# Optimization experiments

Hardware: AMD Instinct MI355X
Metric: run time of the kernel (lower is better)

## Reference

```python
import jax, jax.numpy as jnp
import numpy as np

T, B, D, H = 512, 128, 512, 512

def setup_inputs() -> dict:
    key = jax.random.key(0)
    k1, k2, k3, k4 = jax.random.split(key, 4)
    s_in = 1.0 / np.sqrt(D)
    s_h = 1.0 / np.sqrt(H)
    return {
        "x": jax.random.normal(k1, (T, B, D), dtype=jnp.float32),
        "resets": jax.random.randint(k2, (T, B), 0, 2) > 0,
        "h0": jnp.zeros((B, H), dtype=jnp.float32),  # GRUCell.initialize_carry -> zeros
        "Wi": jax.random.normal(k3, (D, 3 * H), dtype=jnp.float32) * s_in,  # [ir|iz|in]
        "bi": jnp.zeros((3 * H,), dtype=jnp.float32),
        "Wh": jax.random.normal(k4, (H, 3 * H), dtype=jnp.float32) * s_h,  # [hr|hz|hn]
        "bhn": jnp.zeros((H,), dtype=jnp.float32),
    }

def reference(x, resets, h0, Wi, bi, Wh, bhn):
    # Precompute all input-side gate projections in one big GEMM: [T,B,3H]
    xg = jnp.einsum('tbd,dk->tbk', x, Wi) + bi

    def step(h, inp):
        xg_t, reset_t = inp
        # reset masking: replace carry with fresh zero carry where episode resets
        h = jnp.where(reset_t[:, None], jnp.zeros_like(h), h)
        hg = h @ Wh  # [B,3H]
        xr, xz, xn = jnp.split(xg_t, 3, axis=-1)
        hr, hz, hn = jnp.split(hg, 3, axis=-1)
        r = jax.nn.sigmoid(xr + hr)
        z = jax.nn.sigmoid(xz + hz)
        n = jnp.tanh(xn + r * (hn + bhn))
        h_new = (1.0 - z) * n + z * h
        return h_new, h_new

    h_final, ys = jax.lax.scan(step, h0, (xg, resets))
    return h_final, ys
```

## Files before the change

kernel.cpp:

```cpp
#include <hip/hip_runtime.h>

typedef __attribute__((ext_vector_type(4))) float f32x4;
typedef __attribute__((ext_vector_type(8))) _Float16 f16x8;
typedef __attribute__((ext_vector_type(4))) _Float16 f16x4;
typedef unsigned short u16;
typedef unsigned int u32;
typedef unsigned long long u64;

#define XGCAP 34304
#define NXG 4096

__device__ __forceinline__ float sigm(float v){ return 1.0f / (1.0f + __expf(-v)); }
__device__ __forceinline__ float tanh_fast(float v){
  v = fminf(15.0f, fmaxf(-15.0f, v));
  float e = __expf(2.0f * v);
  return (e - 1.0f) / (e + 1.0f);
}
__device__ __forceinline__ void gload16(const void* g, void* l){
  __builtin_amdgcn_global_load_lds((const __attribute__((address_space(1))) void*)g,
                                   (__attribute__((address_space(3))) void*)l, 16, 0, 0);
}
__device__ __forceinline__ double aload(const double* p){
  return __hip_atomic_load(p, __ATOMIC_RELAXED, __HIP_MEMORY_SCOPE_AGENT);
}
__device__ __forceinline__ void astore(float* p, float v){
  __hip_atomic_store(p, v, __ATOMIC_RELAXED, __HIP_MEMORY_SCOPE_AGENT);
}
__device__ __forceinline__ u32 apoll(const u32* p){
  return __hip_atomic_load(p, __ATOMIC_RELAXED, __HIP_MEMORY_SCOPE_AGENT);
}
__device__ __forceinline__ void abump(u32* p, u32 v){
  __hip_atomic_fetch_add(p, v, __ATOMIC_RELAXED, __HIP_MEMORY_SCOPE_AGENT);
}
__device__ __forceinline__ float2 d2f2(double d){ union{double d; float2 f;} u; u.d = d; return u.f; }

__global__ __launch_bounds__(512) void prep_lists(
    const void* __restrict__ resets_raw, const float* __restrict__ h0,
    u32* __restrict__ rows, u32* __restrict__ off, int* __restrict__ nlists)
{
  __shared__ u32 bitmap[2048];
  __shared__ u16 lcnt[127*128];
  __shared__ u32 cnt[520];
  __shared__ u32 offs[521];
  __shared__ u32 cur[520];
  __shared__ int is_bytes, h0nz;
  const int tid = threadIdx.x;
  const int lane = tid & 63, wave = tid >> 6;
  for (int i = tid; i < 2048; i += 512) bitmap[i] = 0;
  for (int i = tid; i < 127*128; i += 512) lcnt[i] = 0;
  for (int i = tid; i < 520; i += 512){ cnt[i] = 0; cur[i] = 0; }
  if (tid == 0){ is_bytes = 0; h0nz = 0; }
  for (int i = tid; i < 64; i += 512) rows[65536 + i] = (2u << 16);
  __syncthreads();
  {
    const u32* w = (const u32*)resets_raw;
    int bad = 0;
    for (int i = tid; i < 4096; i += 512) bad |= (w[i] > 1u);
    if (bad) atomicOr(&is_bytes, 1);
  }
  {
    const u32* hw = (const u32*)h0;
    u32 o = 0;
    for (int i = tid; i < 65536; i += 512) o |= hw[i];
    if (o) atomicOr(&h0nz, 1);
  }
  __syncthreads();
  const bool h0zero = (h0nz == 0);
  if (is_bytes){
    const u32* wb = (const u32*)resets_raw;
    for (int i = tid; i < 16384; i += 512){
      u32 v = wb[i];
      u32 bits = ((v & 0xFFu) ? 1u : 0u) | (((v >> 8) & 0xFFu) ? 2u : 0u)
               | (((v >> 16) & 0xFFu) ? 4u : 0u) | (((v >> 24) & 0xFFu) ? 8u : 0u);
      if (bits) atomicOr(&bitmap[i >> 3], bits << ((i & 7) * 4));
    }
  } else {
    const u32* w = (const u32*)resets_raw;
    for (int r = 0; r < 128; ++r){
      u32 v = w[r * 512 + tid];
      u64 m = __ballot(v != 0u);
      if (lane == 0){
        int idx = r * 16 + wave * 2;
        bitmap[idx] = (u32)m; bitmap[idx + 1] = (u32)(m >> 32);
      }
    }
  }
  __syncthreads();
  if (tid < 128){
    const int b = tid;
    int depth = 0;
    for (int t = 0; t < 512; ++t){
      int pos = t * 128 + b;
      bool rs = (bitmap[pos >> 5] >> (pos & 31)) & 1u;
      depth = rs ? 0 : ((t == 0) ? 0 : depth + 1);
      int li = (depth == 0) ? ((rs || h0zero) ? 0 : 1) : (depth + 1);
      if (li < 127) lcnt[li*128 + b]++;
      else atomicAdd(&cnt[li], 1u);
    }
  }
  __syncthreads();
  if (tid < 127){
    const int li = tid;
    u32 s = 0;
    for (int b = 0; b < 128; ++b){
      u32 v = lcnt[li*128 + b];
      lcnt[li*128 + b] = (u16)s;
      s += v;
    }
    cnt[li] = s;
  }
  __syncthreads();
  if (tid == 0){
    u32 s = 0; int mx = 0;
    for (int i = 0; i < 520; ++i){
      offs[i] = s; s += cnt[i];
      if (cnt[i]) mx = i;
    }
    offs[520] = s;
    *nlists = mx + 1;
  }
  __syncthreads();
  for (int i = tid; i < 521; i += 512) off[i] = offs[i];
  __syncthreads();
  if (tid < 128){
    const int b = tid;
    int depth = 0;
    for (int t = 0; t < 512; ++t){
      int pos = t * 128 + b;
      bool rs = (bitmap[pos >> 5] >> (pos & 31)) & 1u;
      depth = rs ? 0 : ((t == 0) ? 0 : depth + 1);
      int li = (depth == 0) ? ((rs || h0zero) ? 0 : 1) : (depth + 1);
      u32 p;
      if (li < 127){
        u16 c = lcnt[li*128 + b];
        lcnt[li*128 + b] = (u16)(c + 1);
        p = offs[li] + c;
      } else {
        p = offs[li] + atomicAdd(&cur[li], 1u);
      }
      u32 fl = rs ? 1u : ((t == 0) ? (h0zero ? 1u : 2u) : 0u);
      rows[p] = (u32)t | ((u32)b << 9) | (fl << 16);
    }
  }
}

__global__ void prep_w(const float* __restrict__ Wi, const float* __restrict__ Wh,
                       char* __restrict__ wimg, u32* __restrict__ zflags)
{
  if (blockIdx.x < 128){
    #pragma unroll
    for (int i = 0; i < 4; ++i)
      zflags[blockIdx.x * 1024 + (int)threadIdx.x + i * 256] = 0;
  }
  __shared__ float tile[64][65];
  const int bc = blockIdx.x % 24;
  const int bk = blockIdx.x / 24;
  const int scol0 = (bc % 3) * 512 + (bc / 3) * 64;
  const int k0 = bk * 64;
  #pragma unroll
  for (int i = 0; i < 4; ++i){
    int idx = (int)threadIdx.x + i*256;
    int kk = idx >> 4, c4 = idx & 15;
    int k = k0 + kk;
    const float* src = (k < 512) ? (Wi + (size_t)k*1536 + scol0 + c4*4)
                                 : (Wh + (size_t)(k-512)*1536 + scol0 + c4*4);
    float4 v = *(const float4*)src;
    tile[kk][c4*4+0] = v.x; tile[kk][c4*4+1] = v.y;
    tile[kk][c4*4+2] = v.z; tile[kk][c4*4+3] = v.w;
  }
  __syncthreads();
  const int jb = bc / 3;
  #pragma unroll
  for (int i = 0; i < 4; ++i){
    int idx = (int)threadIdx.x + i*256;
    int cc = idx >> 4, k4 = idx & 15;
    int cimg = (bc % 3)*64 + cc;
    f16x4 c;
    c[0] = (_Float16)tile[k4*4+0][cc]; c[1] = (_Float16)tile[k4*4+1][cc];
    c[2] = (_Float16)tile[k4*4+2][cc]; c[3] = (_Float16)tile[k4*4+3][cc];
    int bby = k4*8;
    int sb = (bby & 8) | ((bby & 0x70) ^ ((cimg & 7) << 4));
    *(f16x4*)(wimg + ((size_t)(jb*16 + bk))*24576 + cimg*128 + sb) = c;
  }
}

__global__ __launch_bounds__(256) void prep_x(
    const float* __restrict__ x, const u32* __restrict__ rows,
    char* __restrict__ xq)
{
  const int tid = threadIdx.x;
  const u32 lpos = blockIdx.x * 16 + (tid >> 4);
  const u32 e = rows[lpos];
  const float* src = x + ((size_t)((e & 511u)*128u + ((e >> 9) & 127u)))*512;
  const int lane16 = tid & 15;
  char* dst = xq + (size_t)lpos * 1024;
  const int swzr = ((int)lpos & 7) << 4;
  #pragma unroll
  for (int it = 0; it < 8; ++it){
    float4 v = *(const float4*)(src + it*64 + lane16*4);
    f16x4 c; c[0]=(_Float16)v.x; c[1]=(_Float16)v.y;
             c[2]=(_Float16)v.z; c[3]=(_Float16)v.w;
    int bby = lane16 * 8;
    int sb = (bby & 8) | ((bby & 0x70) ^ swzr);
    *(f16x4*)(dst + it*128 + sb) = c;
  }
}

__global__ __launch_bounds__(256, 2) void gru_fused(
    const char* __restrict__ xq, const float* __restrict__ bi,
    const float* __restrict__ bhn, const char* __restrict__ wimg,
    const float* __restrict__ h0, _Float16* __restrict__ xg,
    const u32* __restrict__ rows, const u32* __restrict__ off,
    const int* __restrict__ nlists, u32* __restrict__ hflags,
    u32* __restrict__ xflags, float* __restrict__ out)
{
  __shared__ __align__(16) char smem[81920];
  float* ys = out + 65536;
  const u32 n0 = off[1];
  const int tid = threadIdx.x;
  const int lane = tid & 63, wave = tid >> 6;
  const int nblk = (int)gridDim.x;

  int g = (int)blockIdx.x;
  while (g < NXG){
    const int tm = g >> 3, jb = g & 7;
    g += nblk;
    const char* asrc = xq + (size_t)tm * 131072;
    const char* wsrc = wimg + ((size_t)jb * 16) * 24576;

    f32x4 acc[3][8];
    #pragma unroll
    for (int c = 0; c < 3; ++c)
      #pragma unroll
      for (int m = 0; m < 8; ++m) acc[c][m] = (f32x4){0.f,0.f,0.f,0.f};

#define DMA_A(KC, BUF) do{ \
    char* l_ = smem + (BUF)*16384 + wave*4096; \
    const char* g_ = asrc + (size_t)(wave*32 + (lane>>3))*1024 + (KC)*128 + (lane&7)*16; \
    _Pragma("unroll") for (int i_ = 0; i_ < 4; ++i_) \
      gload16(g_ + i_*8192, l_ + i_*1024); }while(0)
#define DMA_W(KC, BUF) do{ \
    char* l_ = smem + 32768 + (BUF)*24576 + wave*6144; \
    const char* g_ = wsrc + (size_t)(KC)*24576 + wave*6144 + lane*16; \
    _Pragma("unroll") for (int i_ = 0; i_ < 6; ++i_) \
      gload16(g_ + i_*1024, l_ + i_*1024); }while(0)

    DMA_A(0, 0); DMA_W(0, 0);
    __syncthreads();
    for (int kc = 0; kc < 8; ++kc){
      const int cur = kc & 1;
      if (kc < 7){ DMA_A(kc+1, cur^1); DMA_W(kc+1, cur^1); }
      const char* Ab = smem + cur*16384;
      const char* Wb = smem + 32768 + cur*24576;
      #pragma unroll
      for (int kk = 0; kk < 2; ++kk){
        const int bby = kk*64 + (lane>>4)*16;
        f16x8 af[8];
        #pragma unroll
        for (int mi = 0; mi < 8; ++mi){
          int rr = mi*16 + (lane & 15);
          af[mi] = *(const f16x8*)(Ab + rr*128 + (bby ^ ((rr & 7) << 4)));
        }
        #pragma unroll
        for (int cls = 0; cls < 3; ++cls){
          int cc = cls*64 + wave*16 + (lane & 15);
          f16x8 wf = *(const f16x8*)(Wb + cc*128 + (bby ^ ((cc & 7) << 4)));
          #pragma unroll
          for (int mi = 0; mi < 8; ++mi)
            acc[cls][mi] = __builtin_amdgcn_mfma_f32_16x16x32_f16(af[mi], wf, acc[cls][mi], 0, 0, 0);
        }
      }
      __syncthreads();
    }
#undef DMA_A
#undef DMA_W

    const int jloc = wave*16 + (lane & 15);
    const int j = jb*64 + jloc;
    const float bir = bi[j], biz = bi[512 + j], bin = bi[1024 + j], bh = bhn[j];
    #pragma unroll
    for (int mi = 0; mi < 8; ++mi){
      #pragma unroll
      for (int rg = 0; rg < 4; ++rg){
        int r = mi*16 + (lane >> 4)*4 + rg;
        u32 e = rows[tm*128 + r];
        int tt = (int)(e & 511u), bb = (int)((e >> 9) & 127u);
        float xr = acc[0][mi][rg] + bir;
        float xz = acc[1][mi][rg] + biz;
        float xn = acc[2][mi][rg] + bin;
        if ((e >> 16) == 1u){
          float rr = sigm(xr), zz = sigm(xz);
          float nn = tanh_fast(xn + rr*bh);
          float hv = (1.f - zz)*nn;
          ys[((size_t)(tt*128 + bb))*512 + j] = hv;
          if (tt == 511) out[(size_t)bb*512 + j] = hv;
        } else {
          u32 xi = (u32)(tm*128 + r) - n0;
          if (xi >= XGCAP) xi = 0;
          _Float16* p = xg + (size_t)xi*1536 + jb*192 + jloc;
          p[0]   = (_Float16)xr;
          p[64]  = (_Float16)xz;
          p[128] = (_Float16)xn;
        }
      }
    }
    __syncthreads();
    if (tid < 128){
      u32 e = rows[tm*128 + tid];
      if ((e >> 16) == 1u) abump(&hflags[(e & 511u)*128u + ((e >> 9) & 127u)], 1u);
      else                 abump(&xflags[tm*128 + tid], 1u);
    }
    __syncthreads();
  }

  const int L = *nlists;
  int myNext = g - NXG;
  int gt = 0;
  for (int li = 1; li < L; ++li){
    const u32 offA = off[li];
    const int nA = (int)(off[li+1] - offA);
    const int tA = (nA + 63) >> 6;
    const int nt = tA * 8;
    while (myNext < gt + nt){
      const int tile = myNext - gt;
      myNext += nblk;
      const int tm = tile >> 3, jb = tile & 7;
      const u32 rowbase = offA + (u32)tm*64u;
      const u32 xibase = rowbase - n0;
      const int mcount = min(64, nA - tm*64);
      const char* wp = wimg + ((size_t)jb*16 + 8)*24576;
      const int jloc = wave*16 + (lane & 15);

      if (wave == 0 && lane < mcount){
        u32 e = rows[rowbase + lane];
        const bool needH = ((e >> 16) == 0u);
        u32 hidx = ((e & 511u) - 1u)*128u + ((e >> 9) & 127u);
        int guard = 0;
        for (;;){
          bool ok = apoll(&xflags[rowbase + lane]) >= 8u;
          if (ok && needH) ok = apoll(&hflags[hidx]) >= 8u;
          if (ok) break;
          __builtin_amdgcn_s_sleep(1);
          if (++guard > (1 << 20)) break;
        }
      }
      __syncthreads();

      const float* rp[4];
      #pragma unroll
      for (int i = 0; i < 4; ++i){
        u32 e = rows[rowbase + (tid>>4) + i*16];
        int tt = (int)(e & 511u), bb = (int)((e >> 9) & 127u);
        const float* base = ((e >> 16) == 0u) ? (ys + ((size_t)((tt-1)*128 + bb))*512)
                                              : (h0 + (size_t)bb*512);
        rp[i] = base + (tid & 15)*4;
      }

      _Float16 xgp[3][4][4];
      #pragma unroll
      for (int mi = 0; mi < 4; ++mi){
        #pragma unroll
        for (int rg = 0; rg < 4; ++rg){
          u32 xi = xibase + (u32)(mi*16 + (lane >> 4)*4 + rg);
          if (xi >= XGCAP) xi = 0;
          const _Float16* p = xg + (size_t)xi*1536 + jb*192 + jloc;
          xgp[0][mi][rg] = p[0];
          xgp[1][mi][rg] = p[64];
          xgp[2][mi][rg] = p[128];
        }
      }

      f32x4 acc[3][4];
      #pragma unroll
      for (int c = 0; c < 3; ++c)
        #pragma unroll
        for (int m = 0; m < 4; ++m) acc[c][m] = (f32x4){0.f,0.f,0.f,0.f};
      float hp[4][4];
      double s0[4][2], s1[4][2], s2[4][2];

#define ALOAD(S, CK) do{ \
    _Pragma("unroll") for (int i_ = 0; i_ < 4; ++i_){ \
      const double* p_ = (const double*)(rp[i_] + (CK)*64); \
      S[i_][0] = aload(p_); S[i_][1] = aload(p_ + 1); } }while(0)

#define AWRITE(S, CK) do{ \
    char* An_ = smem + ((CK) & 3)*8192; \
    _Pragma("unroll") for (int i_ = 0; i_ < 4; ++i_){ \
      float2 u0_ = d2f2(S[i_][0]), u1_ = d2f2(S[i_][1]); \
      int r_ = (tid>>4) + i_*16, bby_ = (tid & 15)*8; \
      int sb_ = (bby_ & 8) | ((bby_ & 0x70) ^ ((r_ & 7) << 4)); \
      f16x4 c_; c_[0]=(_Float16)u0_.x; c_[1]=(_Float16)u0_.y; \
                c_[2]=(_Float16)u1_.x; c_[3]=(_Float16)u1_.y; \
      *(f16x4*)(An_ + r_*128 + sb_) = c_; } }while(0)

#define COMPUTE(KC) do{ \
    const char* Ab_ = smem + ((KC) & 3)*8192; \
    _Pragma("unroll") for (int kk_ = 0; kk_ < 2; ++kk_){ \
      const int bby_ = kk_*64 + (lane>>4)*16; \
      f16x8 af_[4]; \
      _Pragma("unroll") for (int mi_ = 0; mi_ < 4; ++mi_){ \
        int rr_ = mi_*16 + (lane & 15); \
        af_[mi_] = *(const f16x8*)(Ab_ + rr_*128 + (bby_ ^ ((rr_ & 7) << 4))); } \
      _Pragma("unroll") for (int cl_ = 0; cl_ < 3; ++cl_){ \
        int cc_ = cl_*64 + wave*16 + (lane & 15); \
        f16x8 wf_ = *(const f16x8*)(wp + (size_t)(KC)*24576 + cc_*128 + (bby_ ^ ((cc_ & 7) << 4))); \
        _Pragma("unroll") for (int mi_ = 0; mi_ < 4; ++mi_) \
          acc[cl_][mi_] = __builtin_amdgcn_mfma_f32_16x16x32_f16(af_[mi_], wf_, acc[cl_][mi_], 0, 0, 0); } } \
    if ((KC) == jb){ \
      const int bb2_ = jloc*2; \
      _Pragma("unroll") for (int mi_ = 0; mi_ < 4; ++mi_) \
        _Pragma("unroll") for (int rg_ = 0; rg_ < 4; ++rg_){ \
          int r2_ = mi_*16 + (lane >> 4)*4 + rg_; \
          int sb2_ = (bb2_ & 0x0F) | ((bb2_ & 0x70) ^ ((r2_ & 7) << 4)); \
          hp[mi_][rg_] = (float)(*(const _Float16*)(Ab_ + r2_*128 + sb2_)); } } }while(0)

      ALOAD(s0, 0); ALOAD(s1, 1); ALOAD(s2, 2);
      AWRITE(s0, 0);
      __syncthreads();
      ALOAD(s0, 3); COMPUTE(0); AWRITE(s1, 1); __syncthreads();
      ALOAD(s1, 4); COMPUTE(1); AWRITE(s2, 2); __syncthreads();
      ALOAD(s2, 5); COMPUTE(2); AWRITE(s0, 3); __syncthreads();
      ALOAD(s0, 6); COMPUTE(3); AWRITE(s1, 4); __syncthreads();
      ALOAD(s1, 7); COMPUTE(4); AWRITE(s2, 5); __syncthreads();
                    COMPUTE(5); AWRITE(s0, 6); __syncthreads();
                    COMPUTE(6); AWRITE(s1, 7); __syncthreads();
                    COMPUTE(7);
#undef ALOAD
#undef AWRITE
#undef COMPUTE

      const int j = jb*64 + jloc;
      const float bh = bhn[j];
      #pragma unroll
      for (int mi = 0; mi < 4; ++mi){
        #pragma unroll
        for (int rg = 0; rg < 4; ++rg){
          int r = mi*16 + (lane >> 4)*4 + rg;
          if (r < mcount){
            u32 e = rows[rowbase + r];
            int tt = (int)(e & 511u), bb = (int)((e >> 9) & 127u);
            float rr = sigm((float)xgp[0][mi][rg] + acc[0][mi][rg]);
            float zz = sigm((float)xgp[1][mi][rg] + acc[1][mi][rg]);
            float nn = tanh_fast((float)xgp[2][mi][rg] + rr*(acc[2][mi][rg] + bh));
            float hv = (1.f - zz)*nn + zz*hp[mi][rg];
            astore(&ys[((size_t)(tt*128 + bb))*512 + j], hv);
            if (tt == 511) out[(size_t)bb*512 + j] = hv;
          }
        }
      }
      __syncthreads();
      if (tid < mcount){
        u32 e = rows[rowbase + tid];
        abump(&hflags[(e & 511u)*128u + ((e >> 9) & 127u)], 1u);
      }
    }
    gt += nt;
  }
}

extern "C" void kernel_launch(void* const* d_in, const int* in_sizes, int n_in,
                              void* d_out, int out_size, void* d_ws, size_t ws_size,
                              hipStream_t stream)
{
  const float* x  = (const float*)d_in[0];
  const void*  resets = d_in[1];
  const float* h0 = (const float*)d_in[2];
  const float* Wi = (const float*)d_in[3];
  const float* bi = (const float*)d_in[4];
  const float* Wh = (const float*)d_in[5];
  const float* bhn= (const float*)d_in[6];
  float* out = (float*)d_out;

  char* ws = (char*)d_ws;
  u32* off    = (u32*)ws;
  int* nlists = (int*)(ws + 4096);
  u32* rows   = (u32*)(ws + 8192);
  u32* hflags = (u32*)(ws + 294912);
  u32* xflags = (u32*)(ws + 557056);
  char* wimg  = ws + 819200;
  char* xq    = ws + 4194304;
  _Float16* xg = (_Float16*)(ws + 71303168);

  prep_lists<<<dim3(1), dim3(512), 0, stream>>>(resets, h0, rows, off, nlists);
  prep_w<<<dim3(384), dim3(256), 0, stream>>>(Wi, Wh, wimg, hflags);
  prep_x<<<dim3(4096), dim3(256), 0, stream>>>(x, rows, xq);

  int perCU = 0;
  (void)hipOccupancyMaxActiveBlocksPerMultiprocessor(&perCU, gru_fused, 256, 0);
  if (perCU < 1) perCU = 1;
  int grid = perCU * 256;
  if (grid > 1024) grid = 1024;

  void* args[] = {(void*)&xq, (void*)&bi, (void*)&bhn, (void*)&wimg,
                  (void*)&h0, (void*)&xg, (void*)&rows, (void*)&off,
                  (void*)&nlists, (void*)&hflags, (void*)&xflags, (void*)&out};
  hipLaunchCooperativeKernel(gru_fused, dim3(grid), dim3(256), args, 0, stream);

  (void)in_sizes; (void)n_in; (void)out_size; (void)ws_size;
}
```

Before: 1.011 ms.

## Double output columns per recurrent tile and parallelize reset-list preprocessing

The recurrent phase now computes two 64-column hidden blocks per tile instead of one. The staged A (previous-hidden) tiles are reused across both weight slices, halving the number of A loads and row-readiness waits per unit of work, and each tile bumps hflags by 2. The cost is double the accumulator and xg register state, which can lower occupancy. The prep_lists kernel is also rewritten so all 512 threads compute per-cell depth from per-column bitmasks with clz, using packed 8-bit counters for small lists instead of a serial 128-thread scan.

```diff
diff --git a/kernel.cpp b/kernel.cpp
--- a/kernel.cpp
+++ b/kernel.cpp
@@ -38,18 +38,16 @@
     const void* __restrict__ resets_raw, const float* __restrict__ h0,
     u32* __restrict__ rows, u32* __restrict__ off, int* __restrict__ nlists)
 {
-  __shared__ u32 bitmap[2048];
-  __shared__ u16 lcnt[127*128];
+  __shared__ u64 cb[128][8];
+  __shared__ u32 cnt8[8][512];
   __shared__ u32 cnt[520];
   __shared__ u32 offs[521];
   __shared__ u32 cur[520];
-  __shared__ int is_bytes, h0nz;
+  __shared__ int is_bytes, h0nz, maxli;
   const int tid = threadIdx.x;
-  const int lane = tid & 63, wave = tid >> 6;
-  for (int i = tid; i < 2048; i += 512) bitmap[i] = 0;
-  for (int i = tid; i < 127*128; i += 512) lcnt[i] = 0;
+  const int b = tid & 127, tc = tid >> 7;
   for (int i = tid; i < 520; i += 512){ cnt[i] = 0; cur[i] = 0; }
-  if (tid == 0){ is_bytes = 0; h0nz = 0; }
+  if (tid == 0){ is_bytes = 0; h0nz = 0; maxli = 0; }
   for (int i = tid; i < 64; i += 512) rows[65536 + i] = (2u << 16);
   __syncthreads();
   {
@@ -66,75 +64,80 @@
   }
   __syncthreads();
   const bool h0zero = (h0nz == 0);
+  u64 bits0 = 0, bits1 = 0;
   if (is_bytes){
-    const u32* wb = (const u32*)resets_raw;
-    for (int i = tid; i < 16384; i += 512){
-      u32 v = wb[i];
-      u32 bits = ((v & 0xFFu) ? 1u : 0u) | (((v >> 8) & 0xFFu) ? 2u : 0u)
-               | (((v >> 16) & 0xFFu) ? 4u : 0u) | (((v >> 24) & 0xFFu) ? 8u : 0u);
-      if (bits) atomicOr(&bitmap[i >> 3], bits << ((i & 7) * 4));
+    const unsigned char* ru8 = (const unsigned char*)resets_raw;
+    for (int i = 0; i < 128; ++i){
+      int t = tc*128 + i;
+      if (ru8[t*128 + b]){
+        if (i < 64) bits0 |= 1ull << i; else bits1 |= 1ull << (i - 64);
+      }
     }
   } else {
-    const u32* w = (const u32*)resets_raw;
-    for (int r = 0; r < 128; ++r){
-      u32 v = w[r * 512 + tid];
-      u64 m = __ballot(v != 0u);
-      if (lane == 0){
-        int idx = r * 16 + wave * 2;
-        bitmap[idx] = (u32)m; bitmap[idx + 1] = (u32)(m >> 32);
-      }
-    }
-  }
-  __syncthreads();
-  if (tid < 128){
-    const int b = tid;
-    int depth = 0;
-    for (int t = 0; t < 512; ++t){
-      int pos = t * 128 + b;
-      bool rs = (bitmap[pos >> 5] >> (pos & 31)) & 1u;
-      depth = rs ? 0 : ((t == 0) ? 0 : depth + 1);
-      int li = (depth == 0) ? ((rs || h0zero) ? 0 : 1) : (depth + 1);
-      if (li < 127) lcnt[li*128 + b]++;
+    const u32* ri32 = (const u32*)resets_raw;
+    for (int i = 0; i < 128; ++i){
+      int t = tc*128 + i;
+      if (ri32[t*128 + b]){
+        if (i < 64) bits0 |= 1ull << i; else bits1 |= 1ull << (i - 64);
+      }
+    }
+  }
+  cb[b][tc*2]     = bits0;
+  cb[b][tc*2 + 1] = bits1;
+  __syncthreads();
+
+#define CELL_LI() \
+    u64 myw = (i < 64) ? bits0 : bits1; \
+    int rs = (int)((myw >> (i & 63)) & 1ull); \
+    int k = t >> 6; \
+    u64 m = cb[b][k] | (k == 0 ? 1ull : 0ull); \
+    int r6 = t & 63; \
+    m &= (r6 == 63) ? ~0ull : ((1ull << (r6 + 1)) - 1ull); \
+    while (m == 0ull){ --k; m = cb[b][k] | (k == 0 ? 1ull : 0ull); } \
+    int lastE = (k << 6) + 63 - (int)__builtin_clzll(m); \
+    int depth = t - lastE; \
+    int li = (depth == 0) ? ((rs || h0zero) ? 0 : 1) : (depth + 1);
+
+  {
+    u64 cpack = 0;
+    int lmax = 0;
+    for (int i = 0; i < 128; ++i){
+      const int t = tc*128 + i;
+      CELL_LI();
+      if (li > lmax) lmax = li;
+      if (li < 8) cpack += 1ull << (li * 8);
       else atomicAdd(&cnt[li], 1u);
     }
-  }
-  __syncthreads();
-  if (tid < 127){
-    const int li = tid;
+    atomicMax(&maxli, lmax);
+    #pragma unroll
+    for (int l = 0; l < 8; ++l) cnt8[l][tid] = (u32)((cpack >> (l * 8)) & 0xFFull);
+  }
+  __syncthreads();
+  if (tid < 8){
     u32 s = 0;
-    for (int b = 0; b < 128; ++b){
-      u32 v = lcnt[li*128 + b];
-      lcnt[li*128 + b] = (u16)s;
-      s += v;
-    }
-    cnt[li] = s;
+    for (int i = 0; i < 512; ++i){ u32 v = cnt8[tid][i]; cnt8[tid][i] = s; s += v; }
+    cnt[tid] = s;
   }
   __syncthreads();
   if (tid == 0){
-    u32 s = 0; int mx = 0;
-    for (int i = 0; i < 520; ++i){
-      offs[i] = s; s += cnt[i];
-      if (cnt[i]) mx = i;
-    }
+    u32 s = 0;
+    for (int i = 0; i < 520; ++i){ offs[i] = s; s += cnt[i]; }
     offs[520] = s;
-    *nlists = mx + 1;
+    *nlists = maxli + 1;
   }
   __syncthreads();
   for (int i = tid; i < 521; i += 512) off[i] = offs[i];
   __syncthreads();
-  if (tid < 128){
-    const int b = tid;
-    int depth = 0;
-    for (int t = 0; t < 512; ++t){
-      int pos = t * 128 + b;
-      bool rs = (bitmap[pos >> 5] >> (pos & 31)) & 1u;
-      depth = rs ? 0 : ((t == 0) ? 0 : depth + 1);
-      int li = (depth == 0) ? ((rs || h0zero) ? 0 : 1) : (depth + 1);
+  {
+    u64 lcpack = 0;
+    for (int i = 0; i < 128; ++i){
+      const int t = tc*128 + i;
+      CELL_LI();
       u32 p;
-      if (li < 127){
-        u16 c = lcnt[li*128 + b];
-        lcnt[li*128 + b] = (u16)(c + 1);
-        p = offs[li] + c;
+      if (li < 8){
+        u32 loc = (u32)((lcpack >> (li * 8)) & 0xFFull);
+        lcpack += 1ull << (li * 8);
+        p = offs[li] + cnt8[li][tid] + loc;
       } else {
         p = offs[li] + atomicAdd(&cur[li], 1u);
       }
@@ -142,6 +145,7 @@
       rows[p] = (u32)t | ((u32)b << 9) | (fl << 16);
     }
   }
+#undef CELL_LI
 }
 
 __global__ void prep_w(const float* __restrict__ Wi, const float* __restrict__ Wh,
@@ -320,15 +324,17 @@
     const u32 offA = off[li];
     const int nA = (int)(off[li+1] - offA);
     const int tA = (nA + 63) >> 6;
-    const int nt = tA * 8;
+    const int nt = tA * 4;
     while (myNext < gt + nt){
       const int tile = myNext - gt;
       myNext += nblk;
-      const int tm = tile >> 3, jb = tile & 7;
+      const int tm = tile >> 2, jp = tile & 3;
+      const int jb0 = jp*2, jb1 = jp*2 + 1;
       const u32 rowbase = offA + (u32)tm*64u;
       const u32 xibase = rowbase - n0;
       const int mcount = min(64, nA - tm*64);
-      const char* wp = wimg + ((size_t)jb*16 + 8)*24576;
+      const char* wp0 = wimg + ((size_t)jb0*16 + 8)*24576;
+      const char* wp1 = wimg + ((size_t)jb1*16 + 8)*24576;
       const int jloc = wave*16 + (lane & 15);
 
       if (wave == 0 && lane < mcount){
@@ -356,26 +362,31 @@
         rp[i] = base + (tid & 15)*4;
       }
 
-      _Float16 xgp[3][4][4];
-      #pragma unroll
-      for (int mi = 0; mi < 4; ++mi){
+      _Float16 xgp[2][3][4][4];
+      #pragma unroll
+      for (int q = 0; q < 2; ++q){
         #pragma unroll
-        for (int rg = 0; rg < 4; ++rg){
-          u32 xi = xibase + (u32)(mi*16 + (lane >> 4)*4 + rg);
-          if (xi >= XGCAP) xi = 0;
-          const _Float16* p = xg + (size_t)xi*1536 + jb*192 + jloc;
-          xgp[0][mi][rg] = p[0];
-          xgp[1][mi][rg] = p[64];
-          xgp[2][mi][rg] = p[128];
+        for (int mi = 0; mi < 4; ++mi){
+          #pragma unroll
+          for (int rg = 0; rg < 4; ++rg){
+            u32 xi = xibase + (u32)(mi*16 + (lane >> 4)*4 + rg);
+            if (xi >= XGCAP) xi = 0;
+            const _Float16* p = xg + (size_t)xi*1536 + (jp*2 + q)*192 + jloc;
+            xgp[q][0][mi][rg] = p[0];
+            xgp[q][1][mi][rg] = p[64];
+            xgp[q][2][mi][rg] = p[128];
+          }
         }
       }
 
-      f32x4 acc[3][4];
-      #pragma unroll
-      for (int c = 0; c < 3; ++c)
+      f32x4 acc[2][3][4];
+      #pragma unroll
+      for (int q = 0; q < 2; ++q)
         #pragma unroll
-        for (int m = 0; m < 4; ++m) acc[c][m] = (f32x4){0.f,0.f,0.f,0.f};
-      float hp[4][4];
+        for (int c = 0; c < 3; ++c)
+          #pragma unroll
+          for (int m = 0; m < 4; ++m) acc[q][c][m] = (f32x4){0.f,0.f,0.f,0.f};
+      _Float16 hp[2][4][4];
       double s0[4][2], s1[4][2], s2[4][2];
 
 #define ALOAD(S, CK) do{ \
@@ -393,6 +404,15 @@
                 c_[2]=(_Float16)u1_.x; c_[3]=(_Float16)u1_.y; \
       *(f16x4*)(An_ + r_*128 + sb_) = c_; } }while(0)
 
+#define CAPTURE_HP(Q, KC) { \
+      const char* Ab2_ = smem + ((KC) & 3)*8192; \
+      const int bb2_ = jloc*2; \
+      _Pragma("unroll") for (int mi_ = 0; mi_ < 4; ++mi_) \
+        _Pragma("unroll") for (int rg_ = 0; rg_ < 4; ++rg_){ \
+          int r2_ = mi_*16 + (lane >> 4)*4 + rg_; \
+          int sb2_ = (bb2_ & 0x0F) | ((bb2_ & 0x70) ^ ((r2_ & 7) << 4)); \
+          hp[Q][mi_][rg_] = *(const _Float16*)(Ab2_ + r2_*128 + sb2_); } }
+
 #define COMPUTE(KC) do{ \
     const char* Ab_ = smem + ((KC) & 3)*8192; \
     _Pragma("unroll") for (int kk_ = 0; kk_ < 2; ++kk_){ \
@@ -401,18 +421,15 @@
       _Pragma("unroll") for (int mi_ = 0; mi_ < 4; ++mi_){ \
         int rr_ = mi_*16 + (lane & 15); \
         af_[mi_] = *(const f16x8*)(Ab_ + rr_*128 + (bby_ ^ ((rr_ & 7) << 4))); } \
-      _Pragma("unroll") for (int cl_ = 0; cl_ < 3; ++cl_){ \
-        int cc_ = cl_*64 + wave*16 + (lane & 15); \
-        f16x8 wf_ = *(const f16x8*)(wp + (size_t)(KC)*24576 + cc_*128 + (bby_ ^ ((cc_ & 7) << 4))); \
-        _Pragma("unroll") for (int mi_ = 0; mi_ < 4; ++mi_) \
-          acc[cl_][mi_] = __builtin_amdgcn_mfma_f32_16x16x32_f16(af_[mi_], wf_, acc[cl_][mi_], 0, 0, 0); } } \
-    if ((KC) == jb){ \
-      const int bb2_ = jloc*2; \
-      _Pragma("unroll") for (int mi_ = 0; mi_ < 4; ++mi_) \
-        _Pragma("unroll") for (int rg_ = 0; rg_ < 4; ++rg_){ \
-          int r2_ = mi_*16 + (lane >> 4)*4 + rg_; \
-          int sb2_ = (bb2_ & 0x0F) | ((bb2_ & 0x70) ^ ((r2_ & 7) << 4)); \
-          hp[mi_][rg_] = (float)(*(const _Float16*)(Ab_ + r2_*128 + sb2_)); } } }while(0)
+      _Pragma("unroll") for (int q_ = 0; q_ < 2; ++q_){ \
+        const char* wpq_ = (q_ == 0) ? wp0 : wp1; \
+        _Pragma("unroll") for (int cl_ = 0; cl_ < 3; ++cl_){ \
+          int cc_ = cl_*64 + wave*16 + (lane & 15); \
+          f16x8 wf_ = *(const f16x8*)(wpq_ + (size_t)(KC)*24576 + cc_*128 + (bby_ ^ ((cc_ & 7) << 4))); \
+          _Pragma("unroll") for (int mi_ = 0; mi_ < 4; ++mi_) \
+            acc[q_][cl_][mi_] = __builtin_amdgcn_mfma_f32_16x16x32_f16(af_[mi_], wf_, acc[q_][cl_][mi_], 0, 0, 0); } } } \
+    if ((KC) == jb0) CAPTURE_HP(0, KC) \
+    if ((KC) == jb1) CAPTURE_HP(1, KC) }while(0)
 
       ALOAD(s0, 0); ALOAD(s1, 1); ALOAD(s2, 2);
       AWRITE(s0, 0);
@@ -428,30 +445,34 @@
 #undef ALOAD
 #undef AWRITE
 #undef COMPUTE
-
-      const int j = jb*64 + jloc;
-      const float bh = bhn[j];
-      #pragma unroll
-      for (int mi = 0; mi < 4; ++mi){
+#undef CAPTURE_HP
+
+      #pragma unroll
+      for (int q = 0; q < 2; ++q){
+        const int j = (jp*2 + q)*64 + jloc;
+        const float bh = bhn[j];
         #pragma unroll
-        for (int rg = 0; rg < 4; ++rg){
-          int r = mi*16 + (lane >> 4)*4 + rg;
-          if (r < mcount){
-            u32 e = rows[rowbase + r];
-            int tt = (int)(e & 511u), bb = (int)((e >> 9) & 127u);
-            float rr = sigm((float)xgp[0][mi][rg] + acc[0][mi][rg]);
-            float zz = sigm((float)xgp[1][mi][rg] + acc[1][mi][rg]);
-            float nn = tanh_fast((float)xgp[2][mi][rg] + rr*(acc[2][mi][rg] + bh));
-            float hv = (1.f - zz)*nn + zz*hp[mi][rg];
-            astore(&ys[((size_t)(tt*128 + bb))*512 + j], hv);
-            if (tt == 511) out[(size_t)bb*512 + j] = hv;
+        for (int mi = 0; mi < 4; ++mi){
+          #pragma unroll
+          for (int rg = 0; rg < 4; ++rg){
+            int r = mi*16 + (lane >> 4)*4 + rg;
+            if (r < mcount){
+              u32 e = rows[rowbase + r];
+              int tt = (int)(e & 511u), bb = (int)((e >> 9) & 127u);
+              float rr = sigm((float)xgp[q][0][mi][rg] + acc[q][0][mi][rg]);
+              float zz = sigm((float)xgp[q][1][mi][rg] + acc[q][1][mi][rg]);
+              float nn = tanh_fast((float)xgp[q][2][mi][rg] + rr*(acc[q][2][mi][rg] + bh));
+              float hv = (1.f - zz)*nn + zz*(float)hp[q][mi][rg];
+              astore(&ys[((size_t)(tt*128 + bb))*512 + j], hv);
+              if (tt == 511) out[(size_t)bb*512 + j] = hv;
+            }
           }
         }
       }
       __syncthreads();
       if (tid < mcount){
         u32 e = rows[rowbase + tid];
-        abump(&hflags[(e & 511u)*128u + ((e >> 9) & 127u)], 1u);
+        abump(&hflags[(e & 511u)*128u + ((e >> 9) & 127u)], 2u);
       }
     }
     gt += nt;
```

New measurement: 1.865 ms. 1.85x slower.
